# Optimization experiments

Hardware: AMD Instinct MI355X
Metric: run time of the kernel (lower is better)

## Reference

```python
import jax, jax.numpy as jnp
import numpy as np

NEG = -1e9  # stand-in for -inf in masked_fill; avoids NaN rows for never-gathered states


def _residual(x, w1, b1, w2, b2):
    # ResidualLayerOld: two relu linears with a residual connection (eval mode, no dropout)
    h = jax.nn.relu(x @ w1.T + b1)
    return x + jax.nn.relu(h @ w2.T + b2)


def setup_inputs() -> dict:
    key = jax.random.key(0)
    B, T, V, C, H, SPW = 16, 256, 32000, 1024, 512, 8
    ks = jax.random.split(key, 32)
    s = 0.05  # keep logits in a sane range
    inp = {
        'start_emb': jax.random.normal(ks[0], (C, H), jnp.float32) * s,
        'start_l1w': jax.random.normal(ks[1], (H, H), jnp.float32) * s,
        'start_l1b': jnp.zeros((H,), jnp.float32),
        'start_l2w': jax.random.normal(ks[2], (H, H), jnp.float32) * s,
        'start_l2b': jnp.zeros((H,), jnp.float32),
        'start_ow': jax.random.normal(ks[3], (1, H), jnp.float32) * s,
        'start_ob': jnp.zeros((1,), jnp.float32),
        'state_emb': jax.random.normal(ks[4], (C, H), jnp.float32) * s,
        'trans_l1w': jax.random.normal(ks[5], (H, H), jnp.float32) * s,
        'trans_l1b': jnp.zeros((H,), jnp.float32),
        'trans_l2w': jax.random.normal(ks[6], (H, H), jnp.float32) * s,
        'trans_l2b': jnp.zeros((H,), jnp.float32),
        'proj_w': jax.random.normal(ks[7], (C, H), jnp.float32) * s,
        'pret_emb': jax.random.normal(ks[8], (C, H), jnp.float32) * s,
        'term_l1w': jax.random.normal(ks[9], (H, H), jnp.float32) * s,
        'term_l1b': jnp.zeros((H,), jnp.float32),
        'term_l2w': jax.random.normal(ks[10], (H, H), jnp.float32) * s,
        'term_l2b': jnp.zeros((H,), jnp.float32),
        'term_ow': jax.random.normal(ks[11], (V, H), jnp.float32) * s,
        'term_ob': jnp.zeros((V,), jnp.float32),
        'text': jax.random.randint(ks[12], (B, T), 0, V, jnp.int32),
        'word2state': jax.random.randint(ks[13], (V, SPW), 0, C, jnp.int32),
    }
    return inp


def reference(start_emb, start_l1w, start_l1b, start_l2w, start_l2b, start_ow, start_ob,
              state_emb, trans_l1w, trans_l1b, trans_l2w, trans_l2b, proj_w,
              pret_emb, term_l1w, term_l1b, term_l2w, term_l2b, term_ow, term_ob,
              text, word2state):
    C, H = start_emb.shape
    V, SPW = word2state.shape

    # start: MLP(C,H)->(C,1) -> log_softmax over C
    start = jax.nn.log_softmax(
        (_residual(start_emb, start_l1w, start_l1b, start_l2w, start_l2b) @ start_ow.T + start_ob).squeeze(-1))

    # transition: [C,C] log_softmax over next state
    trans = jax.nn.log_softmax(
        _residual(state_emb, trans_l1w, trans_l1b, trans_l2w, trans_l2b) @ proj_w.T, axis=-1)

    # emission: [C,V] logits, masked to the sparse word->state assignment, log_softmax over V
    term_logits = _residual(pret_emb, term_l1w, term_l1b, term_l2w, term_l2b) @ term_ow.T + term_ob
    mask = jnp.zeros((C, V), bool).at[word2state.reshape(-1), jnp.repeat(jnp.arange(V), SPW)].set(True)
    emission = jax.nn.log_softmax(jnp.where(mask, term_logits, NEG), axis=-1)

    # clamp: gather per-timestep [SPW,SPW] transition blocks + emissions
    cs = word2state[text]                               # [B,T,SPW]
    pot = trans[cs[:, :-1, :, None], cs[:, 1:, None, :]]  # [B,T-1,SPW,SPW] (prev i, next j)
    init = start[cs[:, 0]]                              # [B,SPW]
    obs = emission[cs, text[:, :, None]]                # [B,T,SPW]
    pot = pot.at[:, 0].add((init + obs[:, 0])[:, :, None])
    pot = pot + obs[:, 1:][:, :, None, :]               # add obs_{t+1} along next-state j
    pot = jnp.swapaxes(pot, -1, -2)                     # [B,T-1,next,prev], as in clamp()

    # forward algorithm (fb kernel's alpha pass): alpha_{t+1}[n] = LSE_p pot[t,n,p] + alpha_t[p]
    def step(alpha, p):
        a = jax.nn.logsumexp(p + alpha[:, None, :], axis=-1)
        return a, None

    B = text.shape[0]
    alpha0 = jnp.zeros((B, SPW), pot.dtype)
    alphaT, _ = jax.lax.scan(step, alpha0, jnp.swapaxes(pot, 0, 1))
    evidence = jax.nn.logsumexp(alphaT, axis=-1).sum()  # full-length sequences
    return evidence
```

## Files before the change

kernel.cpp:

```cpp
#include <hip/hip_runtime.h>
#include <hip/hip_bf16.h>

#define C_DIM 1024
#define H_DIM 512
#define V_DIM 32000
#define B_DIM 16
#define T_DIM 256
#define SPW   8
#define NSLOT 32

typedef unsigned short u16;
typedef unsigned int   u32;
typedef __attribute__((ext_vector_type(8))) short bf16x8;
typedef __attribute__((ext_vector_type(4))) float f32x4;

__device__ __forceinline__ u16 f2b(float f) {
    union { float f; u32 i; } x; x.f = f;
    u32 i = x.i;
    i += 0x7fffu + ((i >> 16) & 1u);
    return (u16)(i >> 16);
}
__device__ __forceinline__ float b2f(u16 u) {
    union { u32 i; float f; } x; x.i = ((u32)u) << 16; return x.f;
}
__device__ __forceinline__ float dot8_bf16(uint4 u, const float4 tw0, const float4 tw1) {
    return tw0.x * b2f((u16)(u.x & 0xffff)) + tw0.y * b2f((u16)(u.x >> 16))
         + tw0.z * b2f((u16)(u.y & 0xffff)) + tw0.w * b2f((u16)(u.y >> 16))
         + tw1.x * b2f((u16)(u.z & 0xffff)) + tw1.y * b2f((u16)(u.z >> 16))
         + tw1.z * b2f((u16)(u.w & 0xffff)) + tw1.w * b2f((u16)(u.w >> 16));
}

struct CvtArgs {
    const float* src[10];
    u16*         dst[10];
    int          n[10];
    float*       zero;
    int          zn;
};

__global__ __launch_bounds__(256) void cvt_kern(CvtArgs a)
{
    int seg = blockIdx.y;
    if (seg == 10) {
        for (int i = blockIdx.x * 256 + threadIdx.x; i < a.zn; i += gridDim.x * 256)
            a.zero[i] = 0.0f;
        return;
    }
    const float4* s = (const float4*)a.src[seg];
    ushort4* d = (ushort4*)a.dst[seg];
    int n4 = a.n[seg] >> 2;
    for (int i = blockIdx.x * 256 + threadIdx.x; i < n4; i += gridDim.x * 256) {
        float4 v = s[i];
        ushort4 o;
        o.x = f2b(v.x); o.y = f2b(v.y); o.z = f2b(v.z); o.w = f2b(v.w);
        d[i] = o;
    }
}

struct Mlp16Args {
    const u16*   A[3];
    const u16*   W[3];
    const float* bias[3];
    const u16*   resid[3];
    u16*         out[3];
};

__global__ __launch_bounds__(256) void mlp16_kern(Mlp16Args args)
{
    const int N = H_DIM, K = H_DIM;
    int z = blockIdx.z;
    const u16* A = args.A[z];
    const u16* B = args.W[z];
    const float* bias = args.bias[z];
    const u16* resid = args.resid[z];
    u16* out = args.out[z];

    __shared__ __align__(16) u16 As[64][40];
    __shared__ __align__(16) u16 Bs[64][40];
    int tid  = threadIdx.x;
    int m0 = blockIdx.x * 64, n0 = blockIdx.y * 64;
    int wave = tid >> 6, lane = tid & 63;
    int wr = wave >> 1, wc = wave & 1;
    int srow = tid >> 2, scol = (tid & 3) << 3;
    int quad = lane >> 4, l16 = lane & 15;
    f32x4 acc[2][2] = {};

    for (int k0 = 0; k0 < K; k0 += 32) {
        uint4 av = *(const uint4*)(A + (size_t)(m0 + srow) * K + k0 + scol);
        uint4 bv = *(const uint4*)(B + (size_t)(n0 + srow) * K + k0 + scol);
        __syncthreads();
        *(uint4*)&As[srow][scol] = av;
        *(uint4*)&Bs[srow][scol] = bv;
        __syncthreads();
        bf16x8 af0 = *(const bf16x8*)&As[wr * 32 + l16][quad * 8];
        bf16x8 af1 = *(const bf16x8*)&As[wr * 32 + 16 + l16][quad * 8];
        bf16x8 bf0 = *(const bf16x8*)&Bs[wc * 32 + l16][quad * 8];
        bf16x8 bf1 = *(const bf16x8*)&Bs[wc * 32 + 16 + l16][quad * 8];
        acc[0][0] = __builtin_amdgcn_mfma_f32_16x16x32_bf16(af0, bf0, acc[0][0], 0, 0, 0);
        acc[0][1] = __builtin_amdgcn_mfma_f32_16x16x32_bf16(af0, bf1, acc[0][1], 0, 0, 0);
        acc[1][0] = __builtin_amdgcn_mfma_f32_16x16x32_bf16(af1, bf0, acc[1][0], 0, 0, 0);
        acc[1][1] = __builtin_amdgcn_mfma_f32_16x16x32_bf16(af1, bf1, acc[1][1], 0, 0, 0);
    }
#pragma unroll
    for (int sm = 0; sm < 2; sm++)
#pragma unroll
        for (int sn = 0; sn < 2; sn++) {
            int n = n0 + wc * 32 + sn * 16 + l16;
            float bv = bias[n];
#pragma unroll
            for (int reg = 0; reg < 4; reg++) {
                int m = m0 + wr * 32 + sm * 16 + quad * 4 + reg;
                float v = fmaxf(acc[sm][sn][reg] + bv, 0.0f);
                if (resid) v += b2f(resid[(size_t)m * N + n]);
                out[(size_t)m * N + n] = f2b(v);
            }
        }
}

__global__ __launch_bounds__(256) void gemm16_kern(
    const u16* __restrict__ A, const u16* __restrict__ B,
    float* __restrict__ out, int M, int N, int K)
{
    __shared__ __align__(16) u16 As[64][40];
    __shared__ __align__(16) u16 Bs[64][40];
    int tid  = threadIdx.x;
    int m0 = blockIdx.x * 64, n0 = blockIdx.y * 64;
    int wave = tid >> 6, lane = tid & 63;
    int wr = wave >> 1, wc = wave & 1;
    int srow = tid >> 2, scol = (tid & 3) << 3;
    int quad = lane >> 4, l16 = lane & 15;
    f32x4 acc[2][2] = {};

    for (int k0 = 0; k0 < K; k0 += 32) {
        uint4 av = *(const uint4*)(A + (size_t)(m0 + srow) * K + k0 + scol);
        uint4 bv = *(const uint4*)(B + (size_t)(n0 + srow) * K + k0 + scol);
        __syncthreads();
        *(uint4*)&As[srow][scol] = av;
        *(uint4*)&Bs[srow][scol] = bv;
        __syncthreads();
        bf16x8 af0 = *(const bf16x8*)&As[wr * 32 + l16][quad * 8];
        bf16x8 af1 = *(const bf16x8*)&As[wr * 32 + 16 + l16][quad * 8];
        bf16x8 bf0 = *(const bf16x8*)&Bs[wc * 32 + l16][quad * 8];
        bf16x8 bf1 = *(const bf16x8*)&Bs[wc * 32 + 16 + l16][quad * 8];
        acc[0][0] = __builtin_amdgcn_mfma_f32_16x16x32_bf16(af0, bf0, acc[0][0], 0, 0, 0);
        acc[0][1] = __builtin_amdgcn_mfma_f32_16x16x32_bf16(af0, bf1, acc[0][1], 0, 0, 0);
        acc[1][0] = __builtin_amdgcn_mfma_f32_16x16x32_bf16(af1, bf0, acc[1][0], 0, 0, 0);
        acc[1][1] = __builtin_amdgcn_mfma_f32_16x16x32_bf16(af1, bf1, acc[1][1], 0, 0, 0);
    }
#pragma unroll
    for (int sm = 0; sm < 2; sm++)
#pragma unroll
        for (int sn = 0; sn < 2; sn++) {
            int n = n0 + wc * 32 + sn * 16 + l16;
#pragma unroll
            for (int reg = 0; reg < 4; reg++) {
                int m = m0 + wr * 32 + sm * 16 + quad * 4 + reg;
                out[(size_t)m * N + n] = acc[sm][sn][reg];
            }
        }
}

__global__ __launch_bounds__(256) void startlog_kern(
    const u16* __restrict__ Rstart16, const float* __restrict__ sow,
    const float* __restrict__ sob, float* __restrict__ startv,
    float* __restrict__ Ssum)
{
    int wid = threadIdx.x >> 6, lane = threadIdx.x & 63;
    int c = blockIdx.x * 4 + wid;
    uint4 rv = ((const uint4*)(Rstart16 + (size_t)c * H_DIM))[lane];
    const float4* wp = (const float4*)(sow);
    float4 w0 = wp[lane * 2], w1 = wp[lane * 2 + 1];
    float d = dot8_bf16(rv, w0, w1);
    for (int off = 1; off < 64; off <<= 1) d += __shfl_xor(d, off, 64);
    if (lane == 0) {
        d += sob[0];
        startv[c] = d;
        atomicAdd(Ssum + (blockIdx.x & (NSLOT - 1)), expf(d));
    }
}

__global__ __launch_bounds__(256) void rowlse_kern(const float* __restrict__ TL,
                                                   float* __restrict__ rowlse)
{
    int wid = threadIdx.x >> 6, lane = threadIdx.x & 63;
    int row = blockIdx.x * 4 + wid;
    const float4* p = (const float4*)(TL + (size_t)row * C_DIM);
    float s = 0.0f;
#pragma unroll
    for (int k = 0; k < 4; k++) {
        float4 v = p[lane + 64 * k];
        s += expf(v.x) + expf(v.y) + expf(v.z) + expf(v.w);
    }
    for (int off = 1; off < 64; off <<= 1) s += __shfl_xor(s, off, 64);
    if (lane == 0) rowlse[row] = logf(s);
}

__global__ __launch_bounds__(256) void zsum_kern(
    const u16* __restrict__ Rterm16, const float* __restrict__ tow,
    const float* __restrict__ tob, const int* __restrict__ w2s,
    float* __restrict__ Zpart)
{
    int wid = threadIdx.x >> 6, lane = threadIdx.x & 63;
    int v = blockIdx.x * 4 + wid;
    float* slot = Zpart + (blockIdx.x & (NSLOT - 1)) * C_DIM;
    const float4* twp = (const float4*)(tow + (size_t)v * H_DIM);
    float4 tw0 = twp[lane * 2], tw1 = twp[lane * 2 + 1];
    float ob = tob[v];
    int cs[SPW];
#pragma unroll
    for (int s = 0; s < SPW; s++) cs[s] = w2s[v * SPW + s];
    uint4 rv[SPW];
#pragma unroll
    for (int s = 0; s < SPW; s++)
        rv[s] = ((const uint4*)(Rterm16 + (size_t)cs[s] * H_DIM))[lane];
    float d[SPW];
#pragma unroll
    for (int s = 0; s < SPW; s++) {
        d[s] = dot8_bf16(rv[s], tw0, tw1);
        d[s] += __shfl_xor(d[s], 1, 64);
        d[s] += __shfl_xor(d[s], 2, 64);
        d[s] += __shfl_xor(d[s], 4, 64);
    }
    float x = d[0];
    int myc = cs[0];
#pragma unroll
    for (int s = 1; s < SPW; s++) {
        if ((lane & 7) == s) { x = d[s]; myc = cs[s]; }
    }
    x += __shfl_xor(x, 8, 64);
    x += __shfl_xor(x, 16, 64);
    x += __shfl_xor(x, 32, 64);
    u32 dupmask = 0;
#pragma unroll
    for (int s = 1; s < SPW; s++) {
        bool dp = false;
#pragma unroll
        for (int s2 = 0; s2 < s; s2++) dp = dp || (cs[s2] == cs[s]);
        if (dp) dupmask |= (1u << s);
    }
    if (lane < 8 && !((dupmask >> lane) & 1u))
        atomicAdd(slot + myc, expf(x + ob));
}

__global__ __launch_bounds__(256) void obs_kern(
    const u16* __restrict__ Rterm16, const float* __restrict__ tow,
    const float* __restrict__ tob, const int* __restrict__ w2s,
    const int* __restrict__ text, const float* __restrict__ Zpart,
    float* __restrict__ obs)
{
    int wid = threadIdx.x >> 6, lane = threadIdx.x & 63;
    int idx = blockIdx.x * 4 + wid;
    int v = text[idx];
    const float4* twp = (const float4*)(tow + (size_t)v * H_DIM);
    float4 tw0 = twp[lane * 2], tw1 = twp[lane * 2 + 1];
    float ob = tob[v];
    int cs[SPW];
#pragma unroll
    for (int s = 0; s < SPW; s++) cs[s] = w2s[v * SPW + s];
    uint4 rv[SPW];
#pragma unroll
    for (int s = 0; s < SPW; s++)
        rv[s] = ((const uint4*)(Rterm16 + (size_t)cs[s] * H_DIM))[lane];
    float d[SPW];
#pragma unroll
    for (int s = 0; s < SPW; s++) {
        d[s] = dot8_bf16(rv[s], tw0, tw1);
        d[s] += __shfl_xor(d[s], 1, 64);
        d[s] += __shfl_xor(d[s], 2, 64);
        d[s] += __shfl_xor(d[s], 4, 64);
    }
    float x = d[0];
    int myc = cs[0];
#pragma unroll
    for (int s = 1; s < SPW; s++) {
        if ((lane & 7) == s) { x = d[s]; myc = cs[s]; }
    }
    x += __shfl_xor(x, 8, 64);
    x += __shfl_xor(x, 16, 64);
    x += __shfl_xor(x, 32, 64);
    int g = lane >> 3;
    float zp = 0.0f;
#pragma unroll
    for (int k = 0; k < 4; k++)
        zp += Zpart[(size_t)(g * 4 + k) * C_DIM + myc];
    zp += __shfl_xor(zp, 8, 64);
    zp += __shfl_xor(zp, 16, 64);
    zp += __shfl_xor(zp, 32, 64);
    if (lane < 8)
        obs[idx * SPW + lane] = x + ob - logf(zp);
}

__device__ __forceinline__ float lsm_combine(float accv, float mv, int i, int j)
{
    float x[8];
#pragma unroll
    for (int k = 0; k < 8; k++) {
        float a = __shfl(accv, k * 8 + i, 64);
        float b = __shfl(mv,  j * 8 + k, 64);
        x[k] = a + b;
    }
    float mx = fmaxf(fmaxf(fmaxf(x[0], x[1]), fmaxf(x[2], x[3])),
                     fmaxf(fmaxf(x[4], x[5]), fmaxf(x[6], x[7])));
    float s = 0.0f;
#pragma unroll
    for (int k = 0; k < 8; k++) s += expf(x[k] - mx);
    return mx + logf(s);
}

__global__ __launch_bounds__(256) void scanA_kern(
    const float* __restrict__ TL, const float* __restrict__ rowlse,
    const float* __restrict__ obs, const float* __restrict__ startv,
    const float* __restrict__ Ssum, const int* __restrict__ text,
    const int* __restrict__ w2s, float* __restrict__ Mc)
{
    int wid = threadIdx.x >> 6, lane = threadIdx.x & 63;
    int g = blockIdx.x * 4 + wid;
    int b = g >> 4, c = g & 15;
    int t0 = c * 16;
    int cnt = min(16, (T_DIM - 1) - t0);
    int i = lane & 7, j = lane >> 3;

    const int* txt = text + b * T_DIM;
    const float* obsb = obs + (size_t)b * T_DIM * SPW;

    float logS = 0.0f;
    if (t0 == 0) {
        float ss = 0.0f;
#pragma unroll
        for (int k = 0; k < NSLOT; k++) ss += Ssum[k];
        logS = logf(ss);
    }

    auto potval = [&](int t) -> float {
        int vt  = txt[t];
        int vt1 = txt[t + 1];
        int ci = w2s[vt * SPW + i];
        int cj = w2s[vt1 * SPW + j];
        float p = TL[(size_t)ci * C_DIM + cj] - rowlse[ci] + obsb[(t + 1) * SPW + j];
        if (t == 0) p += startv[ci] - logS + obsb[i];
        return p;
    };

    float acc = potval(t0);
    if (cnt > 1) {
        float nv = potval(t0 + 1);
        for (int t = t0 + 1; t < t0 + cnt; t++) {
            float nv2 = (t + 1 < t0 + cnt) ? potval(t + 1) : 0.0f;
            acc = lsm_combine(acc, nv, i, j);
            nv = nv2;
        }
    }
    Mc[(size_t)g * 64 + lane] = acc;
}

__global__ __launch_bounds__(1024) void scanB_kern(const float* __restrict__ Mc,
                                                   float* __restrict__ out)
{
    int wave = threadIdx.x >> 6, lane = threadIdx.x & 63;
    int i = lane & 7, j = lane >> 3;
    const float* base = Mc + (size_t)wave * 16 * 64;
    float acc = base[lane];
    for (int c = 1; c < 16; c++)
        acc = lsm_combine(acc, base[(size_t)c * 64 + lane], i, j);
    float mx = acc;
    for (int o = 1; o < 64; o <<= 1) mx = fmaxf(mx, __shfl_xor(mx, o, 64));
    float e = expf(acc - mx);
    for (int o = 1; o < 64; o <<= 1) e += __shfl_xor(e, o, 64);
    __shared__ float part[16];
    if (lane == 0) part[wave] = mx + logf(e);
    __syncthreads();
    if (threadIdx.x == 0) {
        float s = 0.0f;
#pragma unroll
        for (int k = 0; k < 16; k++) s += part[k];
        out[0] = s;
    }
}

extern "C" void kernel_launch(void* const* d_in, const int* in_sizes, int n_in,
                              void* d_out, int out_size, void* d_ws, size_t ws_size,
                              hipStream_t stream)
{
    const float* start_emb = (const float*)d_in[0];
    const float* start_l1w = (const float*)d_in[1];
    const float* start_l1b = (const float*)d_in[2];
    const float* start_l2w = (const float*)d_in[3];
    const float* start_l2b = (const float*)d_in[4];
    const float* start_ow  = (const float*)d_in[5];
    const float* start_ob  = (const float*)d_in[6];
    const float* state_emb = (const float*)d_in[7];
    const float* trans_l1w = (const float*)d_in[8];
    const float* trans_l1b = (const float*)d_in[9];
    const float* trans_l2w = (const float*)d_in[10];
    const float* trans_l2b = (const float*)d_in[11];
    const float* proj_w    = (const float*)d_in[12];
    const float* pret_emb  = (const float*)d_in[13];
    const float* term_l1w  = (const float*)d_in[14];
    const float* term_l1b  = (const float*)d_in[15];
    const float* term_l2w  = (const float*)d_in[16];
    const float* term_l2b  = (const float*)d_in[17];
    const float* term_ow   = (const float*)d_in[18];
    const float* term_ob   = (const float*)d_in[19];
    const int*   text      = (const int*)d_in[20];
    const int*   w2s       = (const int*)d_in[21];

    char* w = (char*)d_ws;
    const u32 MB = 1u << 20;
    const size_t CH = (size_t)C_DIM * H_DIM;
    const size_t HH = (size_t)H_DIM * H_DIM;

    u16* emb16   = (u16*)(w);
    u16* w16     = (u16*)(w + 3u * MB);
    u16* proj16  = (u16*)(w + 6u * MB);
    u16* H16     = (u16*)(w + 7u * MB);
    u16* R16     = (u16*)(w + 10u * MB);
    float* TL    = (float*)(w + 13u * MB);
    float* startv  = (float*)(w + 17u * MB);
    float* rowlse  = (float*)(w + 17u * MB + 4096);
    float* obs     = (float*)(w + 17u * MB + 8192);
    float* Mc      = (float*)(w + 17u * MB + 8192 + 131072);
    float* Zpart   = (float*)(w + 18u * MB);
    float* Ssum    = Zpart + (size_t)NSLOT * C_DIM;

    u16* semb16 = emb16;
    u16* temb16 = emb16 + CH;
    u16* pemb16 = emb16 + 2 * CH;
    u16* sl1w16 = w16;
    u16* sl2w16 = w16 + HH;
    u16* tl1w16 = w16 + 2 * HH;
    u16* tl2w16 = w16 + 3 * HH;
    u16* ml1w16 = w16 + 4 * HH;
    u16* ml2w16 = w16 + 5 * HH;
    u16* Hs = H16, *Ht = H16 + CH, *Hp = H16 + 2 * CH;
    u16* Rstart16 = R16;
    u16* Rtrans16 = R16 + CH;
    u16* Rterm16  = R16 + 2 * CH;

    dim3 blk256(256);

    CvtArgs cv;
    cv.src[0] = start_emb; cv.dst[0] = semb16; cv.n[0] = (int)CH;
    cv.src[1] = state_emb; cv.dst[1] = temb16; cv.n[1] = (int)CH;
    cv.src[2] = pret_emb;  cv.dst[2] = pemb16; cv.n[2] = (int)CH;
    cv.src[3] = start_l1w; cv.dst[3] = sl1w16; cv.n[3] = (int)HH;
    cv.src[4] = start_l2w; cv.dst[4] = sl2w16; cv.n[4] = (int)HH;
    cv.src[5] = trans_l1w; cv.dst[5] = tl1w16; cv.n[5] = (int)HH;
    cv.src[6] = trans_l2w; cv.dst[6] = tl2w16; cv.n[6] = (int)HH;
    cv.src[7] = term_l1w;  cv.dst[7] = ml1w16; cv.n[7] = (int)HH;
    cv.src[8] = term_l2w;  cv.dst[8] = ml2w16; cv.n[8] = (int)HH;
    cv.src[9] = proj_w;    cv.dst[9] = proj16; cv.n[9] = (int)CH;
    cv.zero = Zpart; cv.zn = NSLOT * C_DIM + NSLOT;
    cvt_kern<<<dim3(128, 11), blk256, 0, stream>>>(cv);

    Mlp16Args l1 = {{semb16, temb16, pemb16},
                    {sl1w16, tl1w16, ml1w16},
                    {start_l1b, trans_l1b, term_l1b},
                    {nullptr, nullptr, nullptr},
                    {Hs, Ht, Hp}};
    Mlp16Args l2 = {{Hs, Ht, Hp},
                    {sl2w16, tl2w16, ml2w16},
                    {start_l2b, trans_l2b, term_l2b},
                    {semb16, temb16, pemb16},
                    {Rstart16, Rtrans16, Rterm16}};
    mlp16_kern<<<dim3(16, 8, 3), blk256, 0, stream>>>(l1);
    mlp16_kern<<<dim3(16, 8, 3), blk256, 0, stream>>>(l2);

    gemm16_kern<<<dim3(16, 16), blk256, 0, stream>>>(Rtrans16, proj16, TL,
                                                     C_DIM, C_DIM, H_DIM);

    startlog_kern<<<C_DIM / 4, blk256, 0, stream>>>(Rstart16, start_ow, start_ob,
                                                    startv, Ssum);
    zsum_kern<<<V_DIM / 4, blk256, 0, stream>>>(Rterm16, term_ow, term_ob, w2s, Zpart);
    rowlse_kern<<<C_DIM / 4, blk256, 0, stream>>>(TL, rowlse);
    obs_kern<<<B_DIM * T_DIM / 4, blk256, 0, stream>>>(Rterm16, term_ow, term_ob, w2s,
                                                       text, Zpart, obs);
    scanA_kern<<<B_DIM * 16 / 4, blk256, 0, stream>>>(TL, rowlse, obs, startv, Ssum,
                                                      text, w2s, Mc);
    scanB_kern<<<1, 1024, 0, stream>>>(Mc, (float*)d_out);
}
```

Baseline: 246.0 us.

## Fuse trans GEMM, row-LSE, Z-sum and start logits into one kernel; double-buffer MLP

Merges the transition GEMM, the start-logit dots and the emission Z-sum into a single heterogeneous launch. Row exp-sums are now computed in the GEMM epilogue with atomics, and per-word logits are stored in an Lmat buffer so the separate obs kernel is dropped; scanA reads them directly and subtracts logZ. A small zred kernel finalises the logs. The MLP GEMM gets double-buffered LDS with one sync per k-step, and its residual is read directly from the fp32 embeddings. This cuts launches and removes re-reads of TL and re-computed emission dots, but adds atomics and a mixed-role grid that may load-balance poorly.

```diff
diff --git a/kernel.cpp b/kernel.cpp
--- a/kernel.cpp
+++ b/kernel.cpp
@@ -57,26 +57,26 @@
     }
 }
 
-struct Mlp16Args {
+struct MlpArgs {
     const u16*   A[3];
     const u16*   W[3];
     const float* bias[3];
-    const u16*   resid[3];
+    const float* resid[3];
     u16*         out[3];
 };
 
-__global__ __launch_bounds__(256) void mlp16_kern(Mlp16Args args)
+__global__ __launch_bounds__(256) void mlp16_kern(MlpArgs args)
 {
     const int N = H_DIM, K = H_DIM;
     int z = blockIdx.z;
     const u16* A = args.A[z];
     const u16* B = args.W[z];
     const float* bias = args.bias[z];
-    const u16* resid = args.resid[z];
+    const float* resid = args.resid[z];
     u16* out = args.out[z];
 
-    __shared__ __align__(16) u16 As[64][40];
-    __shared__ __align__(16) u16 Bs[64][40];
+    __shared__ __align__(16) u16 As[2][64][40];
+    __shared__ __align__(16) u16 Bs[2][64][40];
     int tid  = threadIdx.x;
     int m0 = blockIdx.x * 64, n0 = blockIdx.y * 64;
     int wave = tid >> 6, lane = tid & 63;
@@ -85,63 +85,35 @@
     int quad = lane >> 4, l16 = lane & 15;
     f32x4 acc[2][2] = {};
 
-    for (int k0 = 0; k0 < K; k0 += 32) {
-        uint4 av = *(const uint4*)(A + (size_t)(m0 + srow) * K + k0 + scol);
-        uint4 bv = *(const uint4*)(B + (size_t)(n0 + srow) * K + k0 + scol);
-        __syncthreads();
-        *(uint4*)&As[srow][scol] = av;
-        *(uint4*)&Bs[srow][scol] = bv;
-        __syncthreads();
-        bf16x8 af0 = *(const bf16x8*)&As[wr * 32 + l16][quad * 8];
-        bf16x8 af1 = *(const bf16x8*)&As[wr * 32 + 16 + l16][quad * 8];
-        bf16x8 bf0 = *(const bf16x8*)&Bs[wc * 32 + l16][quad * 8];
-        bf16x8 bf1 = *(const bf16x8*)&Bs[wc * 32 + 16 + l16][quad * 8];
+    const u16* ap = A + (size_t)(m0 + srow) * K + scol;
+    const u16* bp = B + (size_t)(n0 + srow) * K + scol;
+
+    *(uint4*)&As[0][srow][scol] = *(const uint4*)ap;
+    *(uint4*)&Bs[0][srow][scol] = *(const uint4*)bp;
+    __syncthreads();
+    int cur = 0;
+#pragma unroll 1
+    for (int k0 = 0; k0 + 32 < K; k0 += 32) {
+        uint4 an = *(const uint4*)(ap + k0 + 32);
+        uint4 bn = *(const uint4*)(bp + k0 + 32);
+        bf16x8 af0 = *(const bf16x8*)&As[cur][wr * 32 + l16][quad * 8];
+        bf16x8 af1 = *(const bf16x8*)&As[cur][wr * 32 + 16 + l16][quad * 8];
+        bf16x8 bf0 = *(const bf16x8*)&Bs[cur][wc * 32 + l16][quad * 8];
+        bf16x8 bf1 = *(const bf16x8*)&Bs[cur][wc * 32 + 16 + l16][quad * 8];
         acc[0][0] = __builtin_amdgcn_mfma_f32_16x16x32_bf16(af0, bf0, acc[0][0], 0, 0, 0);
         acc[0][1] = __builtin_amdgcn_mfma_f32_16x16x32_bf16(af0, bf1, acc[0][1], 0, 0, 0);
         acc[1][0] = __builtin_amdgcn_mfma_f32_16x16x32_bf16(af1, bf0, acc[1][0], 0, 0, 0);
         acc[1][1] = __builtin_amdgcn_mfma_f32_16x16x32_bf16(af1, bf1, acc[1][1], 0, 0, 0);
-    }
-#pragma unroll
-    for (int sm = 0; sm < 2; sm++)
-#pragma unroll
-        for (int sn = 0; sn < 2; sn++) {
-            int n = n0 + wc * 32 + sn * 16 + l16;
-            float bv = bias[n];
-#pragma unroll
-            for (int reg = 0; reg < 4; reg++) {
-                int m = m0 + wr * 32 + sm * 16 + quad * 4 + reg;
-                float v = fmaxf(acc[sm][sn][reg] + bv, 0.0f);
-                if (resid) v += b2f(resid[(size_t)m * N + n]);
-                out[(size_t)m * N + n] = f2b(v);
-            }
-        }
-}
-
-__global__ __launch_bounds__(256) void gemm16_kern(
-    const u16* __restrict__ A, const u16* __restrict__ B,
-    float* __restrict__ out, int M, int N, int K)
-{
-    __shared__ __align__(16) u16 As[64][40];
-    __shared__ __align__(16) u16 Bs[64][40];
-    int tid  = threadIdx.x;
-    int m0 = blockIdx.x * 64, n0 = blockIdx.y * 64;
-    int wave = tid >> 6, lane = tid & 63;
-    int wr = wave >> 1, wc = wave & 1;
-    int srow = tid >> 2, scol = (tid & 3) << 3;
-    int quad = lane >> 4, l16 = lane & 15;
-    f32x4 acc[2][2] = {};
-
-    for (int k0 = 0; k0 < K; k0 += 32) {
-        uint4 av = *(const uint4*)(A + (size_t)(m0 + srow) * K + k0 + scol);
-        uint4 bv = *(const uint4*)(B + (size_t)(n0 + srow) * K + k0 + scol);
+        *(uint4*)&As[cur ^ 1][srow][scol] = an;
+        *(uint4*)&Bs[cur ^ 1][srow][scol] = bn;
         __syncthreads();
-        *(uint4*)&As[srow][scol] = av;
-        *(uint4*)&Bs[srow][scol] = bv;
-        __syncthreads();
-        bf16x8 af0 = *(const bf16x8*)&As[wr * 32 + l16][quad * 8];
-        bf16x8 af1 = *(const bf16x8*)&As[wr * 32 + 16 + l16][quad * 8];
-        bf16x8 bf0 = *(const bf16x8*)&Bs[wc * 32 + l16][quad * 8];
-        bf16x8 bf1 = *(const bf16x8*)&Bs[wc * 32 + 16 + l16][quad * 8];
+        cur ^= 1;
+    }
+    {
+        bf16x8 af0 = *(const bf16x8*)&As[cur][wr * 32 + l16][quad * 8];
+        bf16x8 af1 = *(const bf16x8*)&As[cur][wr * 32 + 16 + l16][quad * 8];
+        bf16x8 bf0 = *(const bf16x8*)&Bs[cur][wc * 32 + l16][quad * 8];
+        bf16x8 bf1 = *(const bf16x8*)&Bs[cur][wc * 32 + 16 + l16][quad * 8];
         acc[0][0] = __builtin_amdgcn_mfma_f32_16x16x32_bf16(af0, bf0, acc[0][0], 0, 0, 0);
         acc[0][1] = __builtin_amdgcn_mfma_f32_16x16x32_bf16(af0, bf1, acc[0][1], 0, 0, 0);
         acc[1][0] = __builtin_amdgcn_mfma_f32_16x16x32_bf16(af1, bf0, acc[1][0], 0, 0, 0);
@@ -152,21 +124,147 @@
 #pragma unroll
         for (int sn = 0; sn < 2; sn++) {
             int n = n0 + wc * 32 + sn * 16 + l16;
+            float bv = bias[n];
 #pragma unroll
             for (int reg = 0; reg < 4; reg++) {
                 int m = m0 + wr * 32 + sm * 16 + quad * 4 + reg;
-                out[(size_t)m * N + n] = acc[sm][sn][reg];
+                float v = fmaxf(acc[sm][sn][reg] + bv, 0.0f);
+                if (resid) v += resid[(size_t)m * N + n];
+                out[(size_t)m * N + n] = f2b(v);
             }
         }
 }
 
-__global__ __launch_bounds__(256) void startlog_kern(
+__global__ __launch_bounds__(256) void fused_mid_kern(
+    const u16* __restrict__ Rtrans16, const u16* __restrict__ proj16,
+    float* __restrict__ TL, float* __restrict__ rowsum,
+    const u16* __restrict__ Rterm16, const float* __restrict__ tow,
+    const float* __restrict__ tob, const int* __restrict__ w2s,
+    float* __restrict__ Zpart, float* __restrict__ Lmat,
     const u16* __restrict__ Rstart16, const float* __restrict__ sow,
     const float* __restrict__ sob, float* __restrict__ startv,
     float* __restrict__ Ssum)
 {
-    int wid = threadIdx.x >> 6, lane = threadIdx.x & 63;
-    int c = blockIdx.x * 4 + wid;
+    __shared__ __align__(16) u16 As[2][64][40];
+    __shared__ __align__(16) u16 Bs[2][64][40];
+    int bx = blockIdx.x;
+    int tid = threadIdx.x;
+    int wid = tid >> 6, lane = tid & 63;
+
+    if (bx < 256) {
+        const int K = H_DIM;
+        int m0 = (bx & 15) * 64, n0 = (bx >> 4) * 64;
+        int wave = wid;
+        int wr = wave >> 1, wc = wave & 1;
+        int srow = tid >> 2, scol = (tid & 3) << 3;
+        int quad = lane >> 4, l16 = lane & 15;
+        f32x4 acc[2][2] = {};
+
+        const u16* ap = Rtrans16 + (size_t)(m0 + srow) * K + scol;
+        const u16* bp = proj16 + (size_t)(n0 + srow) * K + scol;
+
+        *(uint4*)&As[0][srow][scol] = *(const uint4*)ap;
+        *(uint4*)&Bs[0][srow][scol] = *(const uint4*)bp;
+        __syncthreads();
+        int cur = 0;
+#pragma unroll 1
+        for (int k0 = 0; k0 + 32 < K; k0 += 32) {
+            uint4 an = *(const uint4*)(ap + k0 + 32);
+            uint4 bn = *(const uint4*)(bp + k0 + 32);
+            bf16x8 af0 = *(const bf16x8*)&As[cur][wr * 32 + l16][quad * 8];
+            bf16x8 af1 = *(const bf16x8*)&As[cur][wr * 32 + 16 + l16][quad * 8];
+            bf16x8 bf0 = *(const bf16x8*)&Bs[cur][wc * 32 + l16][quad * 8];
+            bf16x8 bf1 = *(const bf16x8*)&Bs[cur][wc * 32 + 16 + l16][quad * 8];
+            acc[0][0] = __builtin_amdgcn_mfma_f32_16x16x32_bf16(af0, bf0, acc[0][0], 0, 0, 0);
+            acc[0][1] = __builtin_amdgcn_mfma_f32_16x16x32_bf16(af0, bf1, acc[0][1], 0, 0, 0);
+            acc[1][0] = __builtin_amdgcn_mfma_f32_16x16x32_bf16(af1, bf0, acc[1][0], 0, 0, 0);
+            acc[1][1] = __builtin_amdgcn_mfma_f32_16x16x32_bf16(af1, bf1, acc[1][1], 0, 0, 0);
+            *(uint4*)&As[cur ^ 1][srow][scol] = an;
+            *(uint4*)&Bs[cur ^ 1][srow][scol] = bn;
+            __syncthreads();
+            cur ^= 1;
+        }
+        {
+            bf16x8 af0 = *(const bf16x8*)&As[cur][wr * 32 + l16][quad * 8];
+            bf16x8 af1 = *(const bf16x8*)&As[cur][wr * 32 + 16 + l16][quad * 8];
+            bf16x8 bf0 = *(const bf16x8*)&Bs[cur][wc * 32 + l16][quad * 8];
+            bf16x8 bf1 = *(const bf16x8*)&Bs[cur][wc * 32 + 16 + l16][quad * 8];
+            acc[0][0] = __builtin_amdgcn_mfma_f32_16x16x32_bf16(af0, bf0, acc[0][0], 0, 0, 0);
+            acc[0][1] = __builtin_amdgcn_mfma_f32_16x16x32_bf16(af0, bf1, acc[0][1], 0, 0, 0);
+            acc[1][0] = __builtin_amdgcn_mfma_f32_16x16x32_bf16(af1, bf0, acc[1][0], 0, 0, 0);
+            acc[1][1] = __builtin_amdgcn_mfma_f32_16x16x32_bf16(af1, bf1, acc[1][1], 0, 0, 0);
+        }
+#pragma unroll
+        for (int sm = 0; sm < 2; sm++)
+#pragma unroll
+            for (int reg = 0; reg < 4; reg++) {
+                int m = m0 + wr * 32 + sm * 16 + quad * 4 + reg;
+                float e = 0.0f;
+#pragma unroll
+                for (int sn = 0; sn < 2; sn++) {
+                    int n = n0 + wc * 32 + sn * 16 + l16;
+                    float v = acc[sm][sn][reg];
+                    TL[(size_t)m * C_DIM + n] = v;
+                    e += expf(v);
+                }
+                e += __shfl_xor(e, 1, 64);
+                e += __shfl_xor(e, 2, 64);
+                e += __shfl_xor(e, 4, 64);
+                e += __shfl_xor(e, 8, 64);
+                if (l16 == 0) atomicAdd(rowsum + m, e);
+            }
+        return;
+    }
+
+    if (bx < 256 + V_DIM / 4) {
+        int vbid = bx - 256;
+        int v = vbid * 4 + wid;
+        float* slot = Zpart + (vbid & (NSLOT - 1)) * C_DIM;
+        const float4* twp = (const float4*)(tow + (size_t)v * H_DIM);
+        float4 tw0 = twp[lane * 2], tw1 = twp[lane * 2 + 1];
+        float ob = tob[v];
+        int cs[SPW];
+#pragma unroll
+        for (int s = 0; s < SPW; s++) cs[s] = w2s[v * SPW + s];
+        uint4 rv[SPW];
+#pragma unroll
+        for (int s = 0; s < SPW; s++)
+            rv[s] = ((const uint4*)(Rterm16 + (size_t)cs[s] * H_DIM))[lane];
+        float d[SPW];
+#pragma unroll
+        for (int s = 0; s < SPW; s++) {
+            d[s] = dot8_bf16(rv[s], tw0, tw1);
+            d[s] += __shfl_xor(d[s], 1, 64);
+            d[s] += __shfl_xor(d[s], 2, 64);
+            d[s] += __shfl_xor(d[s], 4, 64);
+        }
+        float x = d[0];
+        int myc = cs[0];
+#pragma unroll
+        for (int s = 1; s < SPW; s++) {
+            if ((lane & 7) == s) { x = d[s]; myc = cs[s]; }
+        }
+        x += __shfl_xor(x, 8, 64);
+        x += __shfl_xor(x, 16, 64);
+        x += __shfl_xor(x, 32, 64);
+        u32 dupmask = 0;
+#pragma unroll
+        for (int s = 1; s < SPW; s++) {
+            bool dp = false;
+#pragma unroll
+            for (int s2 = 0; s2 < s; s2++) dp = dp || (cs[s2] == cs[s]);
+            if (dp) dupmask |= (1u << s);
+        }
+        if (lane < 8) {
+            Lmat[(size_t)v * SPW + lane] = x + ob;
+            if (!((dupmask >> lane) & 1u))
+                atomicAdd(slot + myc, expf(x + ob));
+        }
+        return;
+    }
+
+    int sbid = bx - (256 + V_DIM / 4);
+    int c = sbid * 4 + wid;
     uint4 rv = ((const uint4*)(Rstart16 + (size_t)c * H_DIM))[lane];
     const float4* wp = (const float4*)(sow);
     float4 w0 = wp[lane * 2], w1 = wp[lane * 2 + 1];
@@ -175,119 +273,20 @@
     if (lane == 0) {
         d += sob[0];
         startv[c] = d;
-        atomicAdd(Ssum + (blockIdx.x & (NSLOT - 1)), expf(d));
-    }
-}
-
-__global__ __launch_bounds__(256) void rowlse_kern(const float* __restrict__ TL,
-                                                   float* __restrict__ rowlse)
-{
-    int wid = threadIdx.x >> 6, lane = threadIdx.x & 63;
-    int row = blockIdx.x * 4 + wid;
-    const float4* p = (const float4*)(TL + (size_t)row * C_DIM);
-    float s = 0.0f;
-#pragma unroll
-    for (int k = 0; k < 4; k++) {
-        float4 v = p[lane + 64 * k];
-        s += expf(v.x) + expf(v.y) + expf(v.z) + expf(v.w);
-    }
-    for (int off = 1; off < 64; off <<= 1) s += __shfl_xor(s, off, 64);
-    if (lane == 0) rowlse[row] = logf(s);
-}
-
-__global__ __launch_bounds__(256) void zsum_kern(
-    const u16* __restrict__ Rterm16, const float* __restrict__ tow,
-    const float* __restrict__ tob, const int* __restrict__ w2s,
-    float* __restrict__ Zpart)
-{
-    int wid = threadIdx.x >> 6, lane = threadIdx.x & 63;
-    int v = blockIdx.x * 4 + wid;
-    float* slot = Zpart + (blockIdx.x & (NSLOT - 1)) * C_DIM;
-    const float4* twp = (const float4*)(tow + (size_t)v * H_DIM);
-    float4 tw0 = twp[lane * 2], tw1 = twp[lane * 2 + 1];
-    float ob = tob[v];
-    int cs[SPW];
-#pragma unroll
-    for (int s = 0; s < SPW; s++) cs[s] = w2s[v * SPW + s];
-    uint4 rv[SPW];
-#pragma unroll
-    for (int s = 0; s < SPW; s++)
-        rv[s] = ((const uint4*)(Rterm16 + (size_t)cs[s] * H_DIM))[lane];
-    float d[SPW];
-#pragma unroll
-    for (int s = 0; s < SPW; s++) {
-        d[s] = dot8_bf16(rv[s], tw0, tw1);
-        d[s] += __shfl_xor(d[s], 1, 64);
-        d[s] += __shfl_xor(d[s], 2, 64);
-        d[s] += __shfl_xor(d[s], 4, 64);
-    }
-    float x = d[0];
-    int myc = cs[0];
-#pragma unroll
-    for (int s = 1; s < SPW; s++) {
-        if ((lane & 7) == s) { x = d[s]; myc = cs[s]; }
-    }
-    x += __shfl_xor(x, 8, 64);
-    x += __shfl_xor(x, 16, 64);
-    x += __shfl_xor(x, 32, 64);
-    u32 dupmask = 0;
-#pragma unroll
-    for (int s = 1; s < SPW; s++) {
-        bool dp = false;
-#pragma unroll
-        for (int s2 = 0; s2 < s; s2++) dp = dp || (cs[s2] == cs[s]);
-        if (dp) dupmask |= (1u << s);
-    }
-    if (lane < 8 && !((dupmask >> lane) & 1u))
-        atomicAdd(slot + myc, expf(x + ob));
-}
-
-__global__ __launch_bounds__(256) void obs_kern(
-    const u16* __restrict__ Rterm16, const float* __restrict__ tow,
-    const float* __restrict__ tob, const int* __restrict__ w2s,
-    const int* __restrict__ text, const float* __restrict__ Zpart,
-    float* __restrict__ obs)
-{
-    int wid = threadIdx.x >> 6, lane = threadIdx.x & 63;
-    int idx = blockIdx.x * 4 + wid;
-    int v = text[idx];
-    const float4* twp = (const float4*)(tow + (size_t)v * H_DIM);
-    float4 tw0 = twp[lane * 2], tw1 = twp[lane * 2 + 1];
-    float ob = tob[v];
-    int cs[SPW];
-#pragma unroll
-    for (int s = 0; s < SPW; s++) cs[s] = w2s[v * SPW + s];
-    uint4 rv[SPW];
-#pragma unroll
-    for (int s = 0; s < SPW; s++)
-        rv[s] = ((const uint4*)(Rterm16 + (size_t)cs[s] * H_DIM))[lane];
-    float d[SPW];
-#pragma unroll
-    for (int s = 0; s < SPW; s++) {
-        d[s] = dot8_bf16(rv[s], tw0, tw1);
-        d[s] += __shfl_xor(d[s], 1, 64);
-        d[s] += __shfl_xor(d[s], 2, 64);
-        d[s] += __shfl_xor(d[s], 4, 64);
-    }
-    float x = d[0];
-    int myc = cs[0];
-#pragma unroll
-    for (int s = 1; s < SPW; s++) {
-        if ((lane & 7) == s) { x = d[s]; myc = cs[s]; }
-    }
-    x += __shfl_xor(x, 8, 64);
-    x += __shfl_xor(x, 16, 64);
-    x += __shfl_xor(x, 32, 64);
-    int g = lane >> 3;
-    float zp = 0.0f;
-#pragma unroll
-    for (int k = 0; k < 4; k++)
-        zp += Zpart[(size_t)(g * 4 + k) * C_DIM + myc];
-    zp += __shfl_xor(zp, 8, 64);
-    zp += __shfl_xor(zp, 16, 64);
-    zp += __shfl_xor(zp, 32, 64);
-    if (lane < 8)
-        obs[idx * SPW + lane] = x + ob - logf(zp);
+        atomicAdd(Ssum + (sbid & (NSLOT - 1)), expf(d));
+    }
+}
+
+__global__ __launch_bounds__(256) void zred_kern(
+    const float* __restrict__ Zpart, const float* __restrict__ rowsum,
+    float* __restrict__ logZ, float* __restrict__ logrow)
+{
+    int c = blockIdx.x * 256 + threadIdx.x;
+    float z = 0.0f;
+#pragma unroll
+    for (int k = 0; k < NSLOT; k++) z += Zpart[(size_t)k * C_DIM + c];
+    logZ[c] = logf(z);
+    logrow[c] = logf(rowsum[c]);
 }
 
 __device__ __forceinline__ float lsm_combine(float accv, float mv, int i, int j)
@@ -307,21 +306,21 @@
     return mx + logf(s);
 }
 
-__global__ __launch_bounds__(256) void scanA_kern(
-    const float* __restrict__ TL, const float* __restrict__ rowlse,
-    const float* __restrict__ obs, const float* __restrict__ startv,
-    const float* __restrict__ Ssum, const int* __restrict__ text,
-    const int* __restrict__ w2s, float* __restrict__ Mc)
-{
-    int wid = threadIdx.x >> 6, lane = threadIdx.x & 63;
-    int g = blockIdx.x * 4 + wid;
+__global__ __launch_bounds__(64) void scanA_kern(
+    const float* __restrict__ TL, const float* __restrict__ logrow,
+    const float* __restrict__ Lmat, const float* __restrict__ logZ,
+    const float* __restrict__ startv, const float* __restrict__ Ssum,
+    const int* __restrict__ text, const int* __restrict__ w2s,
+    float* __restrict__ Mc)
+{
+    int lane = threadIdx.x;
+    int g = blockIdx.x;
     int b = g >> 4, c = g & 15;
     int t0 = c * 16;
     int cnt = min(16, (T_DIM - 1) - t0);
     int i = lane & 7, j = lane >> 3;
 
     const int* txt = text + b * T_DIM;
-    const float* obsb = obs + (size_t)b * T_DIM * SPW;
 
     float logS = 0.0f;
     if (t0 == 0) {
@@ -336,8 +335,10 @@
         int vt1 = txt[t + 1];
         int ci = w2s[vt * SPW + i];
         int cj = w2s[vt1 * SPW + j];
-        float p = TL[(size_t)ci * C_DIM + cj] - rowlse[ci] + obsb[(t + 1) * SPW + j];
-        if (t == 0) p += startv[ci] - logS + obsb[i];
+        float p = TL[(size_t)ci * C_DIM + cj] - logrow[ci]
+                + Lmat[(size_t)vt1 * SPW + j] - logZ[cj];
+        if (t == 0)
+            p += startv[ci] - logS + Lmat[(size_t)vt * SPW + i] - logZ[ci];
         return p;
     };
 
@@ -409,18 +410,20 @@
     const size_t CH = (size_t)C_DIM * H_DIM;
     const size_t HH = (size_t)H_DIM * H_DIM;
 
-    u16* emb16   = (u16*)(w);
-    u16* w16     = (u16*)(w + 3u * MB);
-    u16* proj16  = (u16*)(w + 6u * MB);
-    u16* H16     = (u16*)(w + 7u * MB);
-    u16* R16     = (u16*)(w + 10u * MB);
-    float* TL    = (float*)(w + 13u * MB);
-    float* startv  = (float*)(w + 17u * MB);
-    float* rowlse  = (float*)(w + 17u * MB + 4096);
-    float* obs     = (float*)(w + 17u * MB + 8192);
-    float* Mc      = (float*)(w + 17u * MB + 8192 + 131072);
-    float* Zpart   = (float*)(w + 18u * MB);
-    float* Ssum    = Zpart + (size_t)NSLOT * C_DIM;
+    u16*   emb16  = (u16*)(w);
+    u16*   w16    = (u16*)(w + 3u * MB);
+    u16*   proj16 = (u16*)(w + 6u * MB);
+    u16*   H16    = (u16*)(w + 7u * MB);
+    u16*   R16    = (u16*)(w + 10u * MB);
+    float* TL     = (float*)(w + 13u * MB);
+    float* startv = (float*)(w + 17u * MB);
+    float* logZ   = (float*)(w + 17u * MB + 4096);
+    float* logrow = (float*)(w + 17u * MB + 8192);
+    float* Mc     = (float*)(w + 17u * MB + 12288);
+    float* Zpart  = (float*)(w + 18u * MB);
+    float* Ssum   = Zpart + (size_t)NSLOT * C_DIM;
+    float* rowsum = Ssum + NSLOT;
+    float* Lmat   = (float*)(w + 19u * MB);
 
     u16* semb16 = emb16;
     u16* temb16 = emb16 + CH;
@@ -449,32 +452,34 @@
     cv.src[7] = term_l1w;  cv.dst[7] = ml1w16; cv.n[7] = (int)HH;
     cv.src[8] = term_l2w;  cv.dst[8] = ml2w16; cv.n[8] = (int)HH;
     cv.src[9] = proj_w;    cv.dst[9] = proj16; cv.n[9] = (int)CH;
-    cv.zero = Zpart; cv.zn = NSLOT * C_DIM + NSLOT;
+    cv.zero = Zpart; cv.zn = NSLOT * C_DIM + NSLOT + C_DIM;
     cvt_kern<<<dim3(128, 11), blk256, 0, stream>>>(cv);
 
-    Mlp16Args l1 = {{semb16, temb16, pemb16},
-                    {sl1w16, tl1w16, ml1w16},
-                    {start_l1b, trans_l1b, term_l1b},
-                    {nullptr, nullptr, nullptr},
-                    {Hs, Ht, Hp}};
-    Mlp16Args l2 = {{Hs, Ht, Hp},
-                    {sl2w16, tl2w16, ml2w16},
-                    {start_l2b, trans_l2b, term_l2b},
-                    {semb16, temb16, pemb16},
-                    {Rstart16, Rtrans16, Rterm16}};
+    MlpArgs l1;
+    l1.A[0] = semb16; l1.A[1] = temb16; l1.A[2] = pemb16;
+    l1.W[0] = sl1w16; l1.W[1] = tl1w16; l1.W[2] = ml1w16;
+    l1.bias[0] = start_l1b; l1.bias[1] = trans_l1b; l1.bias[2] = term_l1b;
+    l1.resid[0] = nullptr; l1.resid[1] = nullptr; l1.resid[2] = nullptr;
+    l1.out[0] = Hs; l1.out[1] = Ht; l1.out[2] = Hp;
+
+    MlpArgs l2;
+    l2.A[0] = Hs; l2.A[1] = Ht; l2.A[2] = Hp;
+    l2.W[0] = sl2w16; l2.W[1] = tl2w16; l2.W[2] = ml2w16;
+    l2.bias[0] = start_l2b; l2.bias[1] = trans_l2b; l2.bias[2] = term_l2b;
+    l2.resid[0] = start_emb; l2.resid[1] = state_emb; l2.resid[2] = pret_emb;
+    l2.out[0] = Rstart16; l2.out[1] = Rtrans16; l2.out[2] = Rterm16;
+
     mlp16_kern<<<dim3(16, 8, 3), blk256, 0, stream>>>(l1);
     mlp16_kern<<<dim3(16, 8, 3), blk256, 0, stream>>>(l2);
 
-    gemm16_kern<<<dim3(16, 16), blk256, 0, stream>>>(Rtrans16, proj16, TL,
-                                                     C_DIM, C_DIM, H_DIM);
-
-    startlog_kern<<<C_DIM / 4, blk256, 0, stream>>>(Rstart16, start_ow, start_ob,
-                                                    startv, Ssum);
-    zsum_kern<<<V_DIM / 4, blk256, 0, stream>>>(Rterm16, term_ow, term_ob, w2s, Zpart);
-    rowlse_kern<<<C_DIM / 4, blk256, 0, stream>>>(TL, rowlse);
-    obs_kern<<<B_DIM * T_DIM / 4, blk256, 0, stream>>>(Rterm16, term_ow, term_ob, w2s,
-                                                       text, Zpart, obs);
-    scanA_kern<<<B_DIM * 16 / 4, blk256, 0, stream>>>(TL, rowlse, obs, startv, Ssum,
-                                                      text, w2s, Mc);
+    fused_mid_kern<<<256 + V_DIM / 4 + C_DIM / 4, blk256, 0, stream>>>(
+        Rtrans16, proj16, TL, rowsum,
+        Rterm16, term_ow, term_ob, w2s, Zpart, Lmat,
+        Rstart16, start_ow, start_ob, startv, Ssum);
+
+    zred_kern<<<C_DIM / 256, blk256, 0, stream>>>(Zpart, rowsum, logZ, logrow);
+
+    scanA_kern<<<B_DIM * 16, dim3(64), 0, stream>>>(TL, logrow, Lmat, logZ,
+                                                    startv, Ssum, text, w2s, Mc);
     scanB_kern<<<1, 1024, 0, stream>>>(Mc, (float*)d_out);
 }
```

Measured after the change: 226.0 us. 8.1% less time.
